# Kernel optimization log

Measured on AMD Instinct MI355X. Metric: run time of the kernel, lower is better.

## Reference

```python
import jax, jax.numpy as jnp
import numpy as np

# dims (must match input_specs / init_kwargs)
T, B_SZ, K, OBS_LAST = 512, 8, 128, 2
OBS_DIM = K * OBS_LAST          # 256
N_ACTIONS = 64
N_UNITS, N_FEAT = 256, 8
D_INNER = N_UNITS * N_FEAT      # 2048
H, N_STATE = 16, 64             # p_heads, state_size
P = D_INNER // H                # headdim = 128


def setup_inputs() -> dict:
    key = jax.random.key(0)
    ks = jax.random.split(key, 12)
    s = lambda fan_in: 1.0 / np.sqrt(fan_in)
    return {
        "obs": jax.random.normal(ks[0], (T, B_SZ, K, OBS_LAST), jnp.float32),
        # input projection obs_dim -> d_inner
        "W_in": jax.random.normal(ks[1], (OBS_DIM, D_INNER), jnp.float32) * s(OBS_DIM),
        "b_in": jnp.zeros((D_INNER,), jnp.float32),
        # SSD cell params (Mamba2-style)
        "A_log": jnp.log(jnp.linspace(1.0, 16.0, H).astype(jnp.float32)),
        "dt_bias": jnp.full((H,), -2.0, jnp.float32),
        "W_dt": jax.random.normal(ks[2], (D_INNER, H), jnp.float32) * s(D_INNER),
        "W_B": jax.random.normal(ks[3], (D_INNER, H * N_STATE), jnp.float32) * s(D_INNER),
        "W_C": jax.random.normal(ks[4], (D_INNER, H * N_STATE), jnp.float32) * s(D_INNER),
        # SSD output projection d_inner -> n_units
        "W_yo": jax.random.normal(ks[5], (D_INNER, N_UNITS), jnp.float32) * s(D_INNER),
        "b_yo": jnp.zeros((N_UNITS,), jnp.float32),
        # policy head n_units -> n_actions
        "W_head": jax.random.normal(ks[6], (N_UNITS, N_ACTIONS), jnp.float32) * s(N_UNITS),
        "b_head": jnp.zeros((N_ACTIONS,), jnp.float32),
    }


def _ssd_scan(x, A_log, dt_bias, W_dt, W_B, W_C):
    # x: (T, B, D_INNER) -> y: (T, B, D_INNER) via selective state-space scan
    t, b, _ = x.shape
    dt = jax.nn.softplus(jnp.einsum("tbd,dh->tbh", x, W_dt) + dt_bias)   # (T,B,H)
    Bm = jnp.einsum("tbd,dm->tbm", x, W_B).reshape(t, b, H, N_STATE)      # (T,B,H,N)
    Cm = jnp.einsum("tbd,dm->tbm", x, W_C).reshape(t, b, H, N_STATE)      # (T,B,H,N)
    xh = x.reshape(t, b, H, P)                                            # (T,B,H,P)
    decay = jnp.exp(-jnp.exp(A_log)[None, None, :] * dt)                  # (T,B,H)

    def step(h, inp):
        dec_t, dt_t, B_t, C_t, x_t = inp
        # h: (B,H,P,N); rank-1 input update per head
        h = dec_t[:, :, None, None] * h + dt_t[:, :, None, None] * jnp.einsum(
            "bhp,bhn->bhpn", x_t, B_t)
        y = jnp.einsum("bhpn,bhn->bhp", h, C_t)                           # (B,H,P)
        return h, y

    h0 = jnp.zeros((b, H, P, N_STATE), x.dtype)
    _, ys = jax.lax.scan(step, h0, (decay, dt, Bm, Cm, xh))
    return ys.reshape(t, b, D_INNER)


def reference(obs, W_in, b_in, A_log, dt_bias, W_dt, W_B, W_C, W_yo, b_yo, W_head, b_head):
    t, b = obs.shape[0], obs.shape[1]
    flat = obs.reshape(t * b, -1)                                 # (t*B, obs_dim)
    x = jax.nn.relu(flat @ W_in + b_in).reshape(t, b, D_INNER)     # (t,B,d_inner)
    y = _ssd_scan(x, A_log, dt_bias, W_dt, W_B, W_C)               # (t,B,d_inner)
    hid = jnp.einsum("tbd,du->tbu", y, W_yo) + b_yo                # (t,B,n_units)
    z = jax.nn.relu(hid).reshape(t * b, N_UNITS)
    logits = z @ W_head + b_head
    return logits.reshape(t, b, N_ACTIONS)
```

## Files before the change

### kernel.cpp

```cpp
#include <hip/hip_runtime.h>
#include <cstdint>
#include <cstddef>

typedef unsigned short u16;
typedef __attribute__((ext_vector_type(8))) __bf16 bf16x8;
typedef __attribute__((ext_vector_type(4))) float floatx4;

#define T_DIM   512
#define B_SZ    8
#define ROWS    4096
#define OBS_D   256
#define D_IN    2048
#define NHEAD   16
#define NSTATE  64
#define PDIM    128
#define NUNITS  256
#define NACT    64
#define NSEG    4
#define SEGT    128
#define SLOT    (B_SZ * NHEAD * PDIM * NSTATE)
#define BCSTR   2176
#define BCN     2048

__host__ __device__ __forceinline__ float bf2f(u16 u) {
    union { uint32_t i; float f; } v; v.i = ((uint32_t)u) << 16; return v.f;
}
__host__ __device__ __forceinline__ u16 f2bf(float f) {
    union { float f; uint32_t i; } v; v.f = f;
    uint32_t r = v.i + 0x7FFFu + ((v.i >> 16) & 1u);
    return (u16)(r >> 16);
}

__device__ __forceinline__ void glds16(const u16* g, u16* l) {
    __builtin_amdgcn_global_load_lds(
        (__attribute__((address_space(1))) void*)g,
        (__attribute__((address_space(3))) void*)l, 16, 0, 0);
}

__global__ __launch_bounds__(256) void ActorAgent_27625229647898_kernel(
        float* __restrict__ out, int n, float v) {
    for (int i = blockIdx.x * 256 + threadIdx.x; i < n; i += gridDim.x * 256)
        out[i] = v;
}

__global__ __launch_bounds__(256) void prep(const float* __restrict__ obs,
                                            const float* __restrict__ W_dt,
                                            const float* __restrict__ W_in,
                                            const float* __restrict__ W_B,
                                            const float* __restrict__ W_C,
                                            const float* __restrict__ W_yo,
                                            const float* __restrict__ W_head,
                                            u16* __restrict__ obsb,
                                            u16* __restrict__ WinT, u16* __restrict__ WBCT,
                                            u16* __restrict__ WdtT,
                                            u16* __restrict__ WyoT, u16* __restrict__ WheadT) {
    int bid = blockIdx.x;
    if (bid < 160) {
        const int NOBS = ROWS * OBS_D;
        const int NDT  = D_IN * NHEAD;
        for (int i = bid * 256 + threadIdx.x; i < NOBS + NDT; i += 160 * 256) {
            if (i < NOBS) obsb[i] = f2bf(obs[i]);
            else {
                int j = i - NOBS;
                int k = j >> 4, n = j & 15;
                WdtT[n * D_IN + k] = f2bf(W_dt[j]);
            }
        }
        return;
    }
    bid -= 160;
    const float* src; u16* dst; int R, C, bx, by;
    if (bid < 512)       { src = W_in;   dst = WinT;   R = 256;  C = 2048; bx = bid & 63; by = bid >> 6; }
    else if (bid < 2560) { int i = bid - 512;  src = W_B;  dst = WBCT; R = 2048; C = 1024; bx = i & 31; by = i >> 5; }
    else if (bid < 4608) { int i = bid - 2560; src = W_C;  dst = WBCT + (size_t)1024 * 2048; R = 2048; C = 1024; bx = i & 31; by = i >> 5; }
    else if (bid < 5120) { int i = bid - 4608; src = W_yo; dst = WyoT; R = 2048; C = 256;  bx = i & 7;  by = i >> 3; }
    else                 { int i = bid - 5120; src = W_head; dst = WheadT; R = 256; C = 64; bx = i & 1; by = i >> 1; }
    __shared__ float t[32][33];
    int c0 = bx * 32, r0 = by * 32;
    int tx = threadIdx.x & 31, ty = threadIdx.x >> 5;
#pragma unroll
    for (int i = 0; i < 32; i += 8)
        t[ty + i][tx] = src[(size_t)(r0 + ty + i) * C + c0 + tx];
    __syncthreads();
#pragma unroll
    for (int i = 0; i < 32; i += 8)
        dst[(size_t)(c0 + ty + i) * R + r0 + tx] = f2bf(t[tx][ty + i]);
}

template <int ACT, int OUT_BF16, int HAS_BIAS>
__global__ __launch_bounds__(256) void gemm_bt128(const u16* __restrict__ A,
                                                  const u16* __restrict__ BT,
                                                  const float* __restrict__ bias,
                                                  void* __restrict__ Cout,
                                                  int M, int N, int K, int ldc) {
    __shared__ __align__(16) u16 sA[128 * 32];
    __shared__ __align__(16) u16 sB[128 * 32];
    const int tid  = threadIdx.x;
    const int wave = tid >> 6, lane = tid & 63;
    const int quad = lane >> 4, lr = lane & 15;
    const int wm = wave & 1, wn = wave >> 1;
    const int m0 = blockIdx.x * 128, n0 = blockIdx.y * 128;
    const int r0 = wave * 32 + (lane >> 2);
    const int kel = (lane & 3) * 8;

    floatx4 acc[4][4];
#pragma unroll
    for (int i = 0; i < 4; i++)
#pragma unroll
        for (int j = 0; j < 4; j++)
#pragma unroll
            for (int r = 0; r < 4; r++) acc[i][j][r] = 0.f;

    const u16* apg = A + (size_t)(m0 + r0) * K + kel;
    const u16* bpg = BT + (size_t)(n0 + r0) * K + kel;
    u16* lA0 = &sA[(wave * 32) * 32];
    u16* lA1 = &sA[(wave * 32 + 16) * 32];
    u16* lB0 = &sB[(wave * 32) * 32];
    u16* lB1 = &sB[(wave * 32 + 16) * 32];

    for (int k0 = 0; k0 < K; k0 += 32) {
        __syncthreads();
        glds16(apg + k0, lA0);
        glds16(apg + (size_t)16 * K + k0, lA1);
        glds16(bpg + k0, lB0);
        glds16(bpg + (size_t)16 * K + k0, lB1);
        __syncthreads();
        bf16x8 af[4], bfr[4];
#pragma unroll
        for (int i = 0; i < 4; i++)
            af[i] = *(const bf16x8*)&sA[(wm * 64 + i * 16 + lr) * 32 + quad * 8];
#pragma unroll
        for (int j = 0; j < 4; j++)
            bfr[j] = *(const bf16x8*)&sB[(wn * 64 + j * 16 + lr) * 32 + quad * 8];
#pragma unroll
        for (int i = 0; i < 4; i++)
#pragma unroll
            for (int j = 0; j < 4; j++)
                acc[i][j] = __builtin_amdgcn_mfma_f32_16x16x32_bf16(af[i], bfr[j], acc[i][j], 0, 0, 0);
    }
#pragma unroll
    for (int j = 0; j < 4; j++) {
        int col = n0 + wn * 64 + j * 16 + lr;
        float bvv = HAS_BIAS ? bias[col] : 0.f;
#pragma unroll
        for (int i = 0; i < 4; i++) {
#pragma unroll
            for (int r = 0; r < 4; r++) {
                int row = m0 + wm * 64 + i * 16 + quad * 4 + r;
                float v = acc[i][j][r] + bvv;
                if (ACT) v = fmaxf(v, 0.f);
                if (OUT_BF16) ((u16*)Cout)[(size_t)row * ldc + col] = f2bf(v);
                else          ((float*)Cout)[(size_t)row * ldc + col] = v;
            }
        }
    }
}

template <int ACT, int OUT_BF16>
__global__ __launch_bounds__(256) void gemm_bt64(const u16* __restrict__ A,
                                                 const u16* __restrict__ BT,
                                                 const float* __restrict__ bias,
                                                 void* __restrict__ Cout,
                                                 int M, int N, int K) {
    __shared__ __align__(16) u16 sA[64 * 64];
    __shared__ __align__(16) u16 sB[64 * 64];
    const int tid  = threadIdx.x;
    const int wave = tid >> 6, lane = tid & 63;
    const int quad = lane >> 4, lr = lane & 15;
    const int m0 = blockIdx.x * 64, n0 = blockIdx.y * 64;
    const int srl = lane >> 3, sc = (lane & 7) * 8;

    floatx4 acc[4];
#pragma unroll
    for (int i = 0; i < 4; i++)
#pragma unroll
        for (int j = 0; j < 4; j++) acc[i][j] = 0.f;

    const u16* apg = A + (size_t)(m0 + wave * 16 + srl) * K + sc;
    const u16* bpg = BT + (size_t)(n0 + wave * 16 + srl) * K + sc;

    for (int k0 = 0; k0 < K; k0 += 64) {
        __syncthreads();
#pragma unroll
        for (int g = 0; g < 2; ++g) {
            glds16(apg + (size_t)(g * 8) * K + k0, &sA[(wave * 16 + g * 8) * 64]);
            glds16(bpg + (size_t)(g * 8) * K + k0, &sB[(wave * 16 + g * 8) * 64]);
        }
        __syncthreads();
#pragma unroll
        for (int ks = 0; ks < 2; ++ks) {
            bf16x8 af = *(const bf16x8*)&sA[(wave * 16 + lr) * 64 + ks * 32 + quad * 8];
#pragma unroll
            for (int nt = 0; nt < 4; nt++) {
                bf16x8 bf = *(const bf16x8*)&sB[(nt * 16 + lr) * 64 + ks * 32 + quad * 8];
                acc[nt] = __builtin_amdgcn_mfma_f32_16x16x32_bf16(af, bf, acc[nt], 0, 0, 0);
            }
        }
    }
#pragma unroll
    for (int nt = 0; nt < 4; nt++) {
        int col = n0 + nt * 16 + lr;
        float bvv = bias ? bias[col] : 0.f;
#pragma unroll
        for (int r = 0; r < 4; r++) {
            int row = m0 + wave * 16 + quad * 4 + r;
            float v = acc[nt][r] + bvv;
            if (ACT) v = fmaxf(v, 0.f);
            if (OUT_BF16) ((u16*)Cout)[(size_t)row * N + col] = f2bf(v);
            else          ((float*)Cout)[(size_t)row * N + col] = v;
        }
    }
}

__global__ __launch_bounds__(512) void dtdecay(const u16* __restrict__ xb,
                                               const u16* __restrict__ WdtT,
                                               const float* __restrict__ dt_bias,
                                               const float* __restrict__ A_log,
                                               float* __restrict__ dtv,
                                               float* __restrict__ decayv) {
    __shared__ __align__(16) u16 sw[NHEAD * D_IN];
    const int tid = threadIdx.x;
#pragma unroll
    for (int i = 0; i < 8; ++i) {
        int idx = (tid + i * 512) * 8;
        *(uint4*)&sw[idx] = *(const uint4*)(WdtT + idx);
    }
    __syncthreads();
    const int wave = tid >> 6, lane = tid & 63;
    const int q = lane >> 4, lr = lane & 15;
    const int row = blockIdx.x * 8 + wave;
    const u16* xp = xb + (size_t)row * D_IN;
    float acc[4] = {0.f, 0.f, 0.f, 0.f};
#pragma unroll 4
    for (int k0 = 0; k0 < 16; ++k0) {
        const int kk = k0 * 128 + lr * 8;
        uint4 xv = *(const uint4*)(xp + kk);
        const u16* xu = (const u16*)&xv;
        float xf[8];
#pragma unroll
        for (int j = 0; j < 8; ++j) xf[j] = bf2f(xu[j]);
#pragma unroll
        for (int j = 0; j < 4; ++j) {
            uint4 wv = *(const uint4*)&sw[(q * 4 + j) * D_IN + kk];
            const u16* wu = (const u16*)&wv;
#pragma unroll
            for (int jj = 0; jj < 8; ++jj)
                acc[j] = fmaf(xf[jj], bf2f(wu[jj]), acc[j]);
        }
    }
#pragma unroll
    for (int m = 1; m <= 8; m <<= 1)
#pragma unroll
        for (int j = 0; j < 4; ++j) acc[j] += __shfl_xor(acc[j], m);
    if (lr == 0) {
#pragma unroll
        for (int j = 0; j < 4; ++j) {
            int h = q * 4 + j;
            float z = acc[j] + dt_bias[h];
            float sp = (z > 20.f) ? z : log1pf(expf(z));
            int o = row * NHEAD + h;
            dtv[o] = sp;
            decayv[o] = expf(-expf(A_log[h]) * sp);
        }
    }
}

__global__ __launch_bounds__(256) void seg_state(const u16* __restrict__ xw,
                                                 const u16* __restrict__ BCm,
                                                 const float* __restrict__ dtv,
                                                 const float* __restrict__ decayv,
                                                 float* __restrict__ Hbuf) {
    const int blk = blockIdx.x;
    const int seg = blk >> 7;
    const int b   = (blk >> 4) & 7;
    const int h   = blk & 15;
    const int tid = threadIdx.x;
    const int pgrp = tid >> 3;
    const int oct  = tid & 7;

    __shared__ __align__(16) u16 sx[SEGT][PDIM];
    __shared__ __align__(16) u16 sbm[SEGT][NSTATE];
    __shared__ float sw[SEGT];
    __shared__ float sdt[SEGT];
    __shared__ float sdec[SEGT];
    __shared__ float sP[32];

    const int t0 = seg * SEGT;

#pragma unroll
    for (int k = 0; k < 8; ++k) {
        int idx = tid + k * 256;
        int t = idx >> 4, c = (idx & 15) * 8;
        int r = (t0 + t) * B_SZ + b;
        *(uint4*)&sx[t][c] = *(const uint4*)(xw + (size_t)r * D_IN + h * PDIM + c);
    }
#pragma unroll
    for (int k = 0; k < 4; ++k) {
        int idx = tid + k * 256;
        int t = idx >> 3, c = (idx & 7) * 8;
        int r = (t0 + t) * B_SZ + b;
        *(uint4*)&sbm[t][c] = *(const uint4*)(BCm + (size_t)r * BCSTR + h * NSTATE + c);
    }
    if (tid < SEGT)            sdt[tid] = dtv[((t0 + tid) * B_SZ + b) * NHEAD + h];
    else if (tid < 2 * SEGT)   sdec[tid - SEGT] = decayv[((t0 + tid - SEGT) * B_SZ + b) * NHEAD + h];
    __syncthreads();

    if (tid < 32) {
        float p = 1.f;
        for (int i = 3; i >= 0; --i) {
            int t = tid * 4 + i;
            sw[t] = sdt[t] * p;
            p *= sdec[t];
        }
        sP[tid] = p;
    }
    __syncthreads();
    if (tid == 0) {
        float suf = 1.f;
        for (int q = 31; q >= 0; --q) { float tmp = sP[q]; sP[q] = suf; suf *= tmp; }
    }
    __syncthreads();
    if (tid < 32) {
        float m = sP[tid];
        for (int i = 0; i < 4; ++i) sw[tid * 4 + i] *= m;
    }
    __syncthreads();

    float acc[4][8];
#pragma unroll
    for (int i = 0; i < 4; i++)
#pragma unroll
        for (int j = 0; j < 8; j++) acc[i][j] = 0.f;

    for (int t = 0; t < SEGT; ++t) {
        float w = sw[t];
        const u16* xp = &sx[t][pgrp * 4];
        const u16* bp = &sbm[t][oct * 8];
        float xv[4], bv[8];
#pragma unroll
        for (int i = 0; i < 4; i++) xv[i] = w * bf2f(xp[i]);
#pragma unroll
        for (int j = 0; j < 8; j++) bv[j] = bf2f(bp[j]);
#pragma unroll
        for (int i = 0; i < 4; i++)
#pragma unroll
            for (int j = 0; j < 8; j++)
                acc[i][j] = fmaf(xv[i], bv[j], acc[i][j]);
    }

    float* base = Hbuf + (size_t)seg * SLOT +
                  (((size_t)b * NHEAD + h) * PDIM + pgrp * 4) * NSTATE + oct * 8;
#pragma unroll
    for (int i = 0; i < 4; i++) {
        *(float4*)(base + (size_t)i * NSTATE)     = make_float4(acc[i][0], acc[i][1], acc[i][2], acc[i][3]);
        *(float4*)(base + (size_t)i * NSTATE + 4) = make_float4(acc[i][4], acc[i][5], acc[i][6], acc[i][7]);
    }
}

__global__ __launch_bounds__(256) void seg_prefix(const float* __restrict__ Hbuf,
                                                  const float* __restrict__ decayv,
                                                  u16* __restrict__ Hbf) {
    const int blk = blockIdx.x;
    const int b  = blk >> 6;
    const int h  = (blk >> 2) & 15;
    const int ec = blk & 3;
    const int tid = threadIdx.x;

    __shared__ float sA[NSEG];

    if (tid < 64 * (NSEG - 2)) {
        int s = 1 + (tid >> 6);
        int i = tid & 63;
        int t = s * SEGT + i * 2;
        float p = decayv[(t * B_SZ + b) * NHEAD + h] *
                  decayv[((t + 1) * B_SZ + b) * NHEAD + h];
        p *= __shfl_xor(p, 1);
        p *= __shfl_xor(p, 2);
        p *= __shfl_xor(p, 4);
        p *= __shfl_xor(p, 8);
        p *= __shfl_xor(p, 16);
        p *= __shfl_xor(p, 32);
        if (i == 0) sA[s] = p;
    }
    __syncthreads();

    const size_t base = (((size_t)b * NHEAD + h) * PDIM * NSTATE) + (size_t)ec * 2048 + tid * 8;
    float4 P0 = *(const float4*)(Hbuf + base);
    float4 P1 = *(const float4*)(Hbuf + base + 4);
    u16 pk[8];
    pk[0] = f2bf(P0.x); pk[1] = f2bf(P0.y); pk[2] = f2bf(P0.z); pk[3] = f2bf(P0.w);
    pk[4] = f2bf(P1.x); pk[5] = f2bf(P1.y); pk[6] = f2bf(P1.z); pk[7] = f2bf(P1.w);
    *(uint4*)(Hbf + base) = *(const uint4*)pk;
#pragma unroll
    for (int s = 1; s <= NSEG - 2; ++s) {
        float a = sA[s];
        const float* slot = Hbuf + (size_t)s * SLOT + base;
        float4 h0 = *(const float4*)(slot);
        float4 h1 = *(const float4*)(slot + 4);
        P0.x = fmaf(a, P0.x, h0.x); P0.y = fmaf(a, P0.y, h0.y);
        P0.z = fmaf(a, P0.z, h0.z); P0.w = fmaf(a, P0.w, h0.w);
        P1.x = fmaf(a, P1.x, h1.x); P1.y = fmaf(a, P1.y, h1.y);
        P1.z = fmaf(a, P1.z, h1.z); P1.w = fmaf(a, P1.w, h1.w);
        pk[0] = f2bf(P0.x); pk[1] = f2bf(P0.y); pk[2] = f2bf(P0.z); pk[3] = f2bf(P0.w);
        pk[4] = f2bf(P1.x); pk[5] = f2bf(P1.y); pk[6] = f2bf(P1.z); pk[7] = f2bf(P1.w);
        *(uint4*)(Hbf + (size_t)s * SLOT + base) = *(const uint4*)pk;
    }
}

__global__ __launch_bounds__(256) void chunk_scan(const u16* __restrict__ BCm,
                                                  const float* __restrict__ dtv,
                                                  const float* __restrict__ decayv,
                                                  const u16* __restrict__ Hbf,
                                                  u16* __restrict__ xb) {
    __shared__ __align__(16) u16 sB_[128][68];
    __shared__ __align__(16) u16 sC_[128][68];
    __shared__ __align__(16) u16 sS[128][132];
    __shared__ __align__(16) u16 sXT[128][36];
    __shared__ float sdt[SEGT], sL[SEGT], sEL[SEGT], stmp[32];

    const int blk = blockIdx.x;
    const int seg = blk >> 7, b = (blk >> 4) & 7, h = blk & 15;
    const int tid = threadIdx.x;
    const int wave = tid >> 6, lane = tid & 63;
    const int quad = lane >> 4, lr = lane & 15;
    const int wm = wave & 1, wn = wave >> 1;
    const int t0 = seg * SEGT;

#pragma unroll
    for (int it = 0; it < 4; ++it) {
        int idx = tid + it * 256;
        int t = idx >> 3, c = (idx & 7) * 8;
        int r = (t0 + t) * B_SZ + b;
        *(uint4*)&sB_[t][c] = *(const uint4*)(BCm + (size_t)r * BCSTR + h * NSTATE + c);
        *(uint4*)&sC_[t][c] = *(const uint4*)(BCm + (size_t)r * BCSTR + 1024 + h * NSTATE + c);
    }
    if (tid < SEGT) sdt[tid] = dtv[((t0 + tid) * B_SZ + b) * NHEAD + h];
    else if (tid < 2 * SEGT) {
        int t = tid - SEGT;
        sL[t] = __logf(fmaxf(decayv[((t0 + t) * B_SZ + b) * NHEAD + h], 1e-30f));
    }
    __syncthreads();
    if (tid < 32) {
        float s = 0.f, v[4];
#pragma unroll
        for (int i = 0; i < 4; ++i) { s += sL[tid * 4 + i]; v[i] = s; }
        stmp[tid] = s;
#pragma unroll
        for (int i = 0; i < 4; ++i) sL[tid * 4 + i] = v[i];
    }
    __syncthreads();
    if (tid == 0) {
        float run = 0.f;
        for (int q = 0; q < 32; ++q) { float c2 = stmp[q]; stmp[q] = run; run += c2; }
    }
    __syncthreads();
    if (tid < 32) {
        float off = stmp[tid];
#pragma unroll
        for (int i = 0; i < 4; ++i) sL[tid * 4 + i] += off;
    }
    __syncthreads();
    if (tid < SEGT) sEL[tid] = __expf(sL[tid]);

    floatx4 accS[4][4];
#pragma unroll
    for (int i = 0; i < 4; i++)
#pragma unroll
        for (int j = 0; j < 4; j++)
#pragma unroll
            for (int r = 0; r < 4; r++) accS[i][j][r] = 0.f;
#pragma unroll
    for (int k0 = 0; k0 < 64; k0 += 32) {
        bf16x8 af[4], bfr[4];
#pragma unroll
        for (int i = 0; i < 4; i++)
            af[i] = *(const bf16x8*)&sB_[wm * 64 + i * 16 + lr][k0 + quad * 8];
#pragma unroll
        for (int j = 0; j < 4; j++)
            bfr[j] = *(const bf16x8*)&sC_[wn * 64 + j * 16 + lr][k0 + quad * 8];
#pragma unroll
        for (int i = 0; i < 4; i++)
#pragma unroll
            for (int j = 0; j < 4; j++)
                accS[i][j] = __builtin_amdgcn_mfma_f32_16x16x32_bf16(af[i], bfr[j], accS[i][j], 0, 0, 0);
    }
#pragma unroll
    for (int j = 0; j < 4; j++) {
        int tt = wn * 64 + j * 16 + lr;
        float Lt = sL[tt];
#pragma unroll
        for (int i = 0; i < 4; i++) {
#pragma unroll
            for (int r = 0; r < 4; r++) {
                int tp = wm * 64 + i * 16 + quad * 4 + r;
                float v = 0.f;
                if (tp <= tt) v = accS[i][j][r] * sdt[tp] * __expf(Lt - sL[tp]);
                sS[tt][tp] = f2bf(v);
            }
        }
    }

    floatx4 acc[4][4];
#pragma unroll
    for (int i = 0; i < 4; i++)
#pragma unroll
        for (int j = 0; j < 4; j++)
#pragma unroll
            for (int r = 0; r < 4; r++) acc[i][j][r] = 0.f;
    __syncthreads();
    if (seg > 0) {
        const u16* hbase = Hbf + (size_t)(seg - 1) * SLOT + (((size_t)b * NHEAD + h) * PDIM) * NSTATE;
#pragma unroll
        for (int k0 = 0; k0 < 64; k0 += 32) {
            bf16x8 af[4], bfr[4];
#pragma unroll
            for (int i = 0; i < 4; i++)
                af[i] = *(const bf16x8*)&sC_[wm * 64 + i * 16 + lr][k0 + quad * 8];
#pragma unroll
            for (int j = 0; j < 4; j++)
                bfr[j] = *(const bf16x8*)(hbase + (size_t)(wn * 64 + j * 16 + lr) * NSTATE + k0 + quad * 8);
#pragma unroll
            for (int i = 0; i < 4; i++)
#pragma unroll
                for (int j = 0; j < 4; j++)
                    acc[i][j] = __builtin_amdgcn_mfma_f32_16x16x32_bf16(af[i], bfr[j], acc[i][j], 0, 0, 0);
        }
#pragma unroll
        for (int i = 0; i < 4; i++) {
#pragma unroll
            for (int r = 0; r < 4; r++) {
                float el = sEL[wm * 64 + i * 16 + quad * 4 + r];
#pragma unroll
                for (int j = 0; j < 4; j++) acc[i][j][r] *= el;
            }
        }
    }

    const int px = tid & 127, koh = (tid >> 7) * 16;
    for (int kc = 0; kc < 128; kc += 32) {
        u16 xv[16];
#pragma unroll
        for (int j2 = 0; j2 < 16; ++j2) {
            int tp = kc + koh + j2;
            xv[j2] = xb[(size_t)((t0 + tp) * B_SZ + b) * D_IN + h * PDIM + px];
        }
        __syncthreads();
        *(uint4*)&sXT[px][koh]     = *(const uint4*)&xv[0];
        *(uint4*)&sXT[px][koh + 8] = *(const uint4*)&xv[8];
        __syncthreads();
        bf16x8 af[4], bfr[4];
#pragma unroll
        for (int i = 0; i < 4; i++)
            af[i] = *(const bf16x8*)&sS[wm * 64 + i * 16 + lr][kc + quad * 8];
#pragma unroll
        for (int j = 0; j < 4; j++)
            bfr[j] = *(const bf16x8*)&sXT[wn * 64 + j * 16 + lr][quad * 8];
#pragma unroll
        for (int i = 0; i < 4; i++)
#pragma unroll
            for (int j = 0; j < 4; j++)
                acc[i][j] = __builtin_amdgcn_mfma_f32_16x16x32_bf16(af[i], bfr[j], acc[i][j], 0, 0, 0);
    }

#pragma unroll
    for (int j = 0; j < 4; j++) {
        int p = wn * 64 + j * 16 + lr;
#pragma unroll
        for (int i = 0; i < 4; i++) {
#pragma unroll
            for (int r = 0; r < 4; r++) {
                int t = wm * 64 + i * 16 + quad * 4 + r;
                xb[(size_t)((t0 + t) * B_SZ + b) * D_IN + h * PDIM + p] = f2bf(acc[i][j][r]);
            }
        }
    }
}

extern "C" void kernel_launch(void* const* d_in, const int* in_sizes, int n_in,
                              void* d_out, int out_size, void* d_ws, size_t ws_size,
                              hipStream_t stream) {
    const float* obs     = (const float*)d_in[0];
    const float* W_in    = (const float*)d_in[1];
    const float* b_in    = (const float*)d_in[2];
    const float* A_log   = (const float*)d_in[3];
    const float* dt_bias = (const float*)d_in[4];
    const float* W_dt    = (const float*)d_in[5];
    const float* W_B     = (const float*)d_in[6];
    const float* W_C     = (const float*)d_in[7];
    const float* W_yo    = (const float*)d_in[8];
    const float* b_yo    = (const float*)d_in[9];
    const float* W_head  = (const float*)d_in[10];
    const float* b_head  = (const float*)d_in[11];

    char* ws = (char*)d_ws;
    size_t o = 0;
    u16*   xb     = (u16*)(ws + o);   o += (size_t)ROWS * D_IN * 2;
    u16*   BCm    = (u16*)(ws + o);   o += (size_t)ROWS * BCSTR * 2;
    float* dtv    = (float*)(ws + o); o += (size_t)ROWS * NHEAD * 4;
    float* decayv = (float*)(ws + o); o += (size_t)ROWS * NHEAD * 4;
    u16*   zb     = (u16*)(ws + o);   o += (size_t)ROWS * NUNITS * 2;
    float* Hseg   = (float*)(ws + o); o += (size_t)(NSEG - 1) * SLOT * 4;
    u16*   Hbf    = (u16*)(ws + o);   o += (size_t)(NSEG - 1) * SLOT * 2;
    u16*   obsb   = (u16*)(ws + o);   o += (size_t)ROWS * OBS_D * 2;
    u16*   WinT   = (u16*)(ws + o);   o += (size_t)D_IN * OBS_D * 2;
    u16*   WBCT   = (u16*)(ws + o);   o += (size_t)BCN * D_IN * 2;
    u16*   WdtT   = (u16*)(ws + o);   o += (size_t)NHEAD * D_IN * 2;
    u16*   WyoT   = (u16*)(ws + o);   o += (size_t)NUNITS * D_IN * 2;
    u16*   WheadT = (u16*)(ws + o);   o += (size_t)NACT * NUNITS * 2;

    ActorAgent_27625229647898_kernel<<<dim3(1), 256, 0, stream>>>((float*)d_out, 0, 0.f);

    prep<<<dim3(160 + 5136), 256, 0, stream>>>(obs, W_dt, W_in, W_B, W_C, W_yo, W_head,
                                               obsb, WinT, WBCT, WdtT, WyoT, WheadT);

    gemm_bt128<1, 1, 1><<<dim3(32, 16), 256, 0, stream>>>(obsb, WinT, b_in, xb, ROWS, D_IN, OBS_D, D_IN);
    dtdecay<<<dim3(512), 512, 0, stream>>>(xb, WdtT, dt_bias, A_log, dtv, decayv);
    gemm_bt128<0, 1, 0><<<dim3(32, 16), 256, 0, stream>>>(xb, WBCT, (const float*)nullptr, BCm, ROWS, BCN, D_IN, BCSTR);
    seg_state<<<dim3((NSEG - 1) * 128), 256, 0, stream>>>(xb, BCm, dtv, decayv, Hseg);
    seg_prefix<<<dim3(512), 256, 0, stream>>>(Hseg, decayv, Hbf);
    chunk_scan<<<dim3(NSEG * 128), 256, 0, stream>>>(BCm, dtv, decayv, Hbf, xb);
    gemm_bt64<1, 1><<<dim3(64, 4), 256, 0, stream>>>(xb, WyoT, b_yo, zb, ROWS, NUNITS, D_IN);
    gemm_bt64<0, 0><<<dim3(64, 1), 256, 0, stream>>>(zb, WheadT, b_head, (float*)d_out, ROWS, NACT, NUNITS);
}
```

Measured before the change: 256.4 us.

## Double-buffer LDS tiles in GEMMs and process two rows per wave in dtdecay

Both bf16 MFMA GEMM kernels now use ping-pong LDS buffers. The next K-tile is issued via global-to-LDS loads before computing on the current tile, with one waitcnt plus barrier per iteration instead of two syncthreads. This aims to overlap global load latency with MFMA work, at the cost of twice the LDS per block. Separately, dtdecay has each wave handle two rows and launches half as many blocks, amortizing the 64KB shared weight load per block.

```diff
diff --git a/kernel.cpp b/kernel.cpp
--- a/kernel.cpp
+++ b/kernel.cpp
@@ -93,8 +93,8 @@
                                                   const float* __restrict__ bias,
                                                   void* __restrict__ Cout,
                                                   int M, int N, int K, int ldc) {
-    __shared__ __align__(16) u16 sA[128 * 32];
-    __shared__ __align__(16) u16 sB[128 * 32];
+    __shared__ __align__(16) u16 sA[2][128 * 32];
+    __shared__ __align__(16) u16 sB[2][128 * 32];
     const int tid  = threadIdx.x;
     const int wave = tid >> 6, lane = tid & 63;
     const int quad = lane >> 4, lr = lane & 15;
@@ -113,30 +113,39 @@
 
     const u16* apg = A + (size_t)(m0 + r0) * K + kel;
     const u16* bpg = BT + (size_t)(n0 + r0) * K + kel;
-    u16* lA0 = &sA[(wave * 32) * 32];
-    u16* lA1 = &sA[(wave * 32 + 16) * 32];
-    u16* lB0 = &sB[(wave * 32) * 32];
-    u16* lB1 = &sB[(wave * 32 + 16) * 32];
-
+    const int lofs = (wave * 32) * 32;
+
+    glds16(apg, &sA[0][lofs]);
+    glds16(apg + (size_t)16 * K, &sA[0][lofs + 16 * 32]);
+    glds16(bpg, &sB[0][lofs]);
+    glds16(bpg + (size_t)16 * K, &sB[0][lofs + 16 * 32]);
+    asm volatile("s_waitcnt vmcnt(0)" ::: "memory");
+    __builtin_amdgcn_s_barrier();
+
+    int cur = 0;
     for (int k0 = 0; k0 < K; k0 += 32) {
-        __syncthreads();
-        glds16(apg + k0, lA0);
-        glds16(apg + (size_t)16 * K + k0, lA1);
-        glds16(bpg + k0, lB0);
-        glds16(bpg + (size_t)16 * K + k0, lB1);
-        __syncthreads();
+        if (k0 + 32 < K) {
+            int nb = cur ^ 1;
+            glds16(apg + k0 + 32, &sA[nb][lofs]);
+            glds16(apg + (size_t)16 * K + k0 + 32, &sA[nb][lofs + 16 * 32]);
+            glds16(bpg + k0 + 32, &sB[nb][lofs]);
+            glds16(bpg + (size_t)16 * K + k0 + 32, &sB[nb][lofs + 16 * 32]);
+        }
         bf16x8 af[4], bfr[4];
 #pragma unroll
         for (int i = 0; i < 4; i++)
-            af[i] = *(const bf16x8*)&sA[(wm * 64 + i * 16 + lr) * 32 + quad * 8];
+            af[i] = *(const bf16x8*)&sA[cur][(wm * 64 + i * 16 + lr) * 32 + quad * 8];
 #pragma unroll
         for (int j = 0; j < 4; j++)
-            bfr[j] = *(const bf16x8*)&sB[(wn * 64 + j * 16 + lr) * 32 + quad * 8];
+            bfr[j] = *(const bf16x8*)&sB[cur][(wn * 64 + j * 16 + lr) * 32 + quad * 8];
 #pragma unroll
         for (int i = 0; i < 4; i++)
 #pragma unroll
             for (int j = 0; j < 4; j++)
                 acc[i][j] = __builtin_amdgcn_mfma_f32_16x16x32_bf16(af[i], bfr[j], acc[i][j], 0, 0, 0);
+        asm volatile("s_waitcnt vmcnt(0)" ::: "memory");
+        __builtin_amdgcn_s_barrier();
+        cur ^= 1;
     }
 #pragma unroll
     for (int j = 0; j < 4; j++) {
@@ -162,8 +171,8 @@
                                                  const float* __restrict__ bias,
                                                  void* __restrict__ Cout,
                                                  int M, int N, int K) {
-    __shared__ __align__(16) u16 sA[64 * 64];
-    __shared__ __align__(16) u16 sB[64 * 64];
+    __shared__ __align__(16) u16 sA[2][64 * 64];
+    __shared__ __align__(16) u16 sB[2][64 * 64];
     const int tid  = threadIdx.x;
     const int wave = tid >> 6, lane = tid & 63;
     const int quad = lane >> 4, lr = lane & 15;
@@ -179,23 +188,36 @@
     const u16* apg = A + (size_t)(m0 + wave * 16 + srl) * K + sc;
     const u16* bpg = BT + (size_t)(n0 + wave * 16 + srl) * K + sc;
 
+#pragma unroll
+    for (int g = 0; g < 2; ++g) {
+        glds16(apg + (size_t)(g * 8) * K, &sA[0][(wave * 16 + g * 8) * 64]);
+        glds16(bpg + (size_t)(g * 8) * K, &sB[0][(wave * 16 + g * 8) * 64]);
+    }
+    asm volatile("s_waitcnt vmcnt(0)" ::: "memory");
+    __builtin_amdgcn_s_barrier();
+
+    int cur = 0;
     for (int k0 = 0; k0 < K; k0 += 64) {
-        __syncthreads();
-#pragma unroll
-        for (int g = 0; g < 2; ++g) {
-            glds16(apg + (size_t)(g * 8) * K + k0, &sA[(wave * 16 + g * 8) * 64]);
-            glds16(bpg + (size_t)(g * 8) * K + k0, &sB[(wave * 16 + g * 8) * 64]);
-        }
-        __syncthreads();
+        if (k0 + 64 < K) {
+            int nb = cur ^ 1;
+#pragma unroll
+            for (int g = 0; g < 2; ++g) {
+                glds16(apg + (size_t)(g * 8) * K + k0 + 64, &sA[nb][(wave * 16 + g * 8) * 64]);
+                glds16(bpg + (size_t)(g * 8) * K + k0 + 64, &sB[nb][(wave * 16 + g * 8) * 64]);
+            }
+        }
 #pragma unroll
         for (int ks = 0; ks < 2; ++ks) {
-            bf16x8 af = *(const bf16x8*)&sA[(wave * 16 + lr) * 64 + ks * 32 + quad * 8];
+            bf16x8 af = *(const bf16x8*)&sA[cur][(wave * 16 + lr) * 64 + ks * 32 + quad * 8];
 #pragma unroll
             for (int nt = 0; nt < 4; nt++) {
-                bf16x8 bf = *(const bf16x8*)&sB[(nt * 16 + lr) * 64 + ks * 32 + quad * 8];
+                bf16x8 bf = *(const bf16x8*)&sB[cur][(nt * 16 + lr) * 64 + ks * 32 + quad * 8];
                 acc[nt] = __builtin_amdgcn_mfma_f32_16x16x32_bf16(af, bf, acc[nt], 0, 0, 0);
             }
         }
+        asm volatile("s_waitcnt vmcnt(0)" ::: "memory");
+        __builtin_amdgcn_s_barrier();
+        cur ^= 1;
     }
 #pragma unroll
     for (int nt = 0; nt < 4; nt++) {
@@ -228,39 +250,42 @@
     __syncthreads();
     const int wave = tid >> 6, lane = tid & 63;
     const int q = lane >> 4, lr = lane & 15;
-    const int row = blockIdx.x * 8 + wave;
-    const u16* xp = xb + (size_t)row * D_IN;
-    float acc[4] = {0.f, 0.f, 0.f, 0.f};
+#pragma unroll 1
+    for (int rr = 0; rr < 2; ++rr) {
+        const int row = blockIdx.x * 16 + wave * 2 + rr;
+        const u16* xp = xb + (size_t)row * D_IN;
+        float acc[4] = {0.f, 0.f, 0.f, 0.f};
 #pragma unroll 4
-    for (int k0 = 0; k0 < 16; ++k0) {
-        const int kk = k0 * 128 + lr * 8;
-        uint4 xv = *(const uint4*)(xp + kk);
-        const u16* xu = (const u16*)&xv;
-        float xf[8];
-#pragma unroll
-        for (int j = 0; j < 8; ++j) xf[j] = bf2f(xu[j]);
-#pragma unroll
-        for (int j = 0; j < 4; ++j) {
-            uint4 wv = *(const uint4*)&sw[(q * 4 + j) * D_IN + kk];
-            const u16* wu = (const u16*)&wv;
-#pragma unroll
-            for (int jj = 0; jj < 8; ++jj)
-                acc[j] = fmaf(xf[jj], bf2f(wu[jj]), acc[j]);
-        }
-    }
-#pragma unroll
-    for (int m = 1; m <= 8; m <<= 1)
-#pragma unroll
-        for (int j = 0; j < 4; ++j) acc[j] += __shfl_xor(acc[j], m);
-    if (lr == 0) {
-#pragma unroll
-        for (int j = 0; j < 4; ++j) {
-            int h = q * 4 + j;
-            float z = acc[j] + dt_bias[h];
-            float sp = (z > 20.f) ? z : log1pf(expf(z));
-            int o = row * NHEAD + h;
-            dtv[o] = sp;
-            decayv[o] = expf(-expf(A_log[h]) * sp);
+        for (int k0 = 0; k0 < 16; ++k0) {
+            const int kk = k0 * 128 + lr * 8;
+            uint4 xv = *(const uint4*)(xp + kk);
+            const u16* xu = (const u16*)&xv;
+            float xf[8];
+#pragma unroll
+            for (int j = 0; j < 8; ++j) xf[j] = bf2f(xu[j]);
+#pragma unroll
+            for (int j = 0; j < 4; ++j) {
+                uint4 wv = *(const uint4*)&sw[(q * 4 + j) * D_IN + kk];
+                const u16* wu = (const u16*)&wv;
+#pragma unroll
+                for (int jj = 0; jj < 8; ++jj)
+                    acc[j] = fmaf(xf[jj], bf2f(wu[jj]), acc[j]);
+            }
+        }
+#pragma unroll
+        for (int m = 1; m <= 8; m <<= 1)
+#pragma unroll
+            for (int j = 0; j < 4; ++j) acc[j] += __shfl_xor(acc[j], m);
+        if (lr == 0) {
+#pragma unroll
+            for (int j = 0; j < 4; ++j) {
+                int h = q * 4 + j;
+                float z = acc[j] + dt_bias[h];
+                float sp = (z > 20.f) ? z : log1pf(expf(z));
+                int o = row * NHEAD + h;
+                dtv[o] = sp;
+                decayv[o] = expf(-expf(A_log[h]) * sp);
+            }
         }
     }
 }
@@ -614,7 +639,7 @@
                                                obsb, WinT, WBCT, WdtT, WyoT, WheadT);
 
     gemm_bt128<1, 1, 1><<<dim3(32, 16), 256, 0, stream>>>(obsb, WinT, b_in, xb, ROWS, D_IN, OBS_D, D_IN);
-    dtdecay<<<dim3(512), 512, 0, stream>>>(xb, WdtT, dt_bias, A_log, dtv, decayv);
+    dtdecay<<<dim3(256), 512, 0, stream>>>(xb, WdtT, dt_bias, A_log, dtv, decayv);
     gemm_bt128<0, 1, 0><<<dim3(32, 16), 256, 0, stream>>>(xb, WBCT, (const float*)nullptr, BCm, ROWS, BCN, D_IN, BCSTR);
     seg_state<<<dim3((NSEG - 1) * 128), 256, 0, stream>>>(xb, BCm, dtv, decayv, Hseg);
     seg_prefix<<<dim3(512), 256, 0, stream>>>(Hseg, decayv, Hbf);
```

Result: no change. 255.1 us (-0.5%).

## Triple-buffer GEMM LDS loads and process two rows per wave in dtdecay

Applied to the files above, without the earlier changes.

Both GEMM kernels move to a three-stage LDS ring. Global-to-LDS loads are issued two k-tiles ahead and guarded by explicit vmcnt waits and raw barriers, so memory latency overlaps with the MFMA work. The dtdecay kernel now has each wave compute two rows, which reuses each shared-memory weight read and halves the grid. This costs more LDS per block, which may lower occupancy, and the hand-placed waitcnt counts assume each glds16 issues exactly one vm op.

```diff
diff --git a/kernel.cpp b/kernel.cpp
--- a/kernel.cpp
+++ b/kernel.cpp
@@ -93,8 +93,8 @@
                                                   const float* __restrict__ bias,
                                                   void* __restrict__ Cout,
                                                   int M, int N, int K, int ldc) {
-    __shared__ __align__(16) u16 sA[128 * 32];
-    __shared__ __align__(16) u16 sB[128 * 32];
+    __shared__ __align__(16) u16 sA[3][128 * 32];
+    __shared__ __align__(16) u16 sB[3][128 * 32];
     const int tid  = threadIdx.x;
     const int wave = tid >> 6, lane = tid & 63;
     const int quad = lane >> 4, lr = lane & 15;
@@ -113,31 +113,49 @@
 
     const u16* apg = A + (size_t)(m0 + r0) * K + kel;
     const u16* bpg = BT + (size_t)(n0 + r0) * K + kel;
-    u16* lA0 = &sA[(wave * 32) * 32];
-    u16* lA1 = &sA[(wave * 32 + 16) * 32];
-    u16* lB0 = &sB[(wave * 32) * 32];
-    u16* lB1 = &sB[(wave * 32 + 16) * 32];
-
-    for (int k0 = 0; k0 < K; k0 += 32) {
-        __syncthreads();
-        glds16(apg + k0, lA0);
-        glds16(apg + (size_t)16 * K + k0, lA1);
-        glds16(bpg + k0, lB0);
-        glds16(bpg + (size_t)16 * K + k0, lB1);
-        __syncthreads();
+    const int lofs = (wave * 32) * 32;
+    const int ntk = K >> 5;
+
+#define STAGE128(t, sb) do {                                        \
+        int kk_ = (t) << 5;                                         \
+        glds16(apg + kk_, &sA[sb][lofs]);                           \
+        glds16(apg + (size_t)16 * K + kk_, &sA[sb][lofs + 16 * 32]);\
+        glds16(bpg + kk_, &sB[sb][lofs]);                           \
+        glds16(bpg + (size_t)16 * K + kk_, &sB[sb][lofs + 16 * 32]);\
+    } while (0)
+
+    STAGE128(0, 0);
+    STAGE128(1, 1);
+    int s = 0;
+    for (int t = 0; t < ntk; ++t) {
+        if (t + 2 < ntk) {
+            int ns = s + 2; if (ns >= 3) ns -= 3;
+            STAGE128(t + 2, ns);
+            asm volatile("s_waitcnt vmcnt(8)" ::: "memory");
+        } else if (t + 1 < ntk) {
+            asm volatile("s_waitcnt vmcnt(4)" ::: "memory");
+        } else {
+            asm volatile("s_waitcnt vmcnt(0)" ::: "memory");
+        }
+        __builtin_amdgcn_s_barrier();
+        asm volatile("" ::: "memory");
         bf16x8 af[4], bfr[4];
 #pragma unroll
         for (int i = 0; i < 4; i++)
-            af[i] = *(const bf16x8*)&sA[(wm * 64 + i * 16 + lr) * 32 + quad * 8];
+            af[i] = *(const bf16x8*)&sA[s][(wm * 64 + i * 16 + lr) * 32 + quad * 8];
 #pragma unroll
         for (int j = 0; j < 4; j++)
-            bfr[j] = *(const bf16x8*)&sB[(wn * 64 + j * 16 + lr) * 32 + quad * 8];
+            bfr[j] = *(const bf16x8*)&sB[s][(wn * 64 + j * 16 + lr) * 32 + quad * 8];
 #pragma unroll
         for (int i = 0; i < 4; i++)
 #pragma unroll
             for (int j = 0; j < 4; j++)
                 acc[i][j] = __builtin_amdgcn_mfma_f32_16x16x32_bf16(af[i], bfr[j], acc[i][j], 0, 0, 0);
-    }
+        asm volatile("" ::: "memory");
+        __builtin_amdgcn_s_barrier();
+        ++s; if (s == 3) s = 0;
+    }
+#undef STAGE128
 #pragma unroll
     for (int j = 0; j < 4; j++) {
         int col = n0 + wn * 64 + j * 16 + lr;
@@ -162,8 +180,8 @@
                                                  const float* __restrict__ bias,
                                                  void* __restrict__ Cout,
                                                  int M, int N, int K) {
-    __shared__ __align__(16) u16 sA[64 * 64];
-    __shared__ __align__(16) u16 sB[64 * 64];
+    __shared__ __align__(16) u16 sA[3][64 * 64];
+    __shared__ __align__(16) u16 sB[3][64 * 64];
     const int tid  = threadIdx.x;
     const int wave = tid >> 6, lane = tid & 63;
     const int quad = lane >> 4, lr = lane & 15;
@@ -178,25 +196,45 @@
 
     const u16* apg = A + (size_t)(m0 + wave * 16 + srl) * K + sc;
     const u16* bpg = BT + (size_t)(n0 + wave * 16 + srl) * K + sc;
-
-    for (int k0 = 0; k0 < K; k0 += 64) {
-        __syncthreads();
-#pragma unroll
-        for (int g = 0; g < 2; ++g) {
-            glds16(apg + (size_t)(g * 8) * K + k0, &sA[(wave * 16 + g * 8) * 64]);
-            glds16(bpg + (size_t)(g * 8) * K + k0, &sB[(wave * 16 + g * 8) * 64]);
-        }
-        __syncthreads();
+    const int ntk = K >> 6;
+
+#define STAGE64(t, sb) do {                                            \
+        int kk_ = (t) << 6;                                            \
+        glds16(apg + kk_,                 &sA[sb][(wave * 16) * 64]);  \
+        glds16(apg + (size_t)8 * K + kk_, &sA[sb][(wave * 16 + 8) * 64]);\
+        glds16(bpg + kk_,                 &sB[sb][(wave * 16) * 64]);  \
+        glds16(bpg + (size_t)8 * K + kk_, &sB[sb][(wave * 16 + 8) * 64]);\
+    } while (0)
+
+    STAGE64(0, 0);
+    STAGE64(1, 1);
+    int s = 0;
+    for (int t = 0; t < ntk; ++t) {
+        if (t + 2 < ntk) {
+            int ns = s + 2; if (ns >= 3) ns -= 3;
+            STAGE64(t + 2, ns);
+            asm volatile("s_waitcnt vmcnt(8)" ::: "memory");
+        } else if (t + 1 < ntk) {
+            asm volatile("s_waitcnt vmcnt(4)" ::: "memory");
+        } else {
+            asm volatile("s_waitcnt vmcnt(0)" ::: "memory");
+        }
+        __builtin_amdgcn_s_barrier();
+        asm volatile("" ::: "memory");
 #pragma unroll
         for (int ks = 0; ks < 2; ++ks) {
-            bf16x8 af = *(const bf16x8*)&sA[(wave * 16 + lr) * 64 + ks * 32 + quad * 8];
+            bf16x8 af = *(const bf16x8*)&sA[s][(wave * 16 + lr) * 64 + ks * 32 + quad * 8];
 #pragma unroll
             for (int nt = 0; nt < 4; nt++) {
-                bf16x8 bf = *(const bf16x8*)&sB[(nt * 16 + lr) * 64 + ks * 32 + quad * 8];
+                bf16x8 bf = *(const bf16x8*)&sB[s][(nt * 16 + lr) * 64 + ks * 32 + quad * 8];
                 acc[nt] = __builtin_amdgcn_mfma_f32_16x16x32_bf16(af, bf, acc[nt], 0, 0, 0);
             }
         }
-    }
+        asm volatile("" ::: "memory");
+        __builtin_amdgcn_s_barrier();
+        ++s; if (s == 3) s = 0;
+    }
+#undef STAGE64
 #pragma unroll
     for (int nt = 0; nt < 4; nt++) {
         int col = n0 + nt * 16 + lr;
@@ -228,39 +266,53 @@
     __syncthreads();
     const int wave = tid >> 6, lane = tid & 63;
     const int q = lane >> 4, lr = lane & 15;
-    const int row = blockIdx.x * 8 + wave;
-    const u16* xp = xb + (size_t)row * D_IN;
-    float acc[4] = {0.f, 0.f, 0.f, 0.f};
+    const int row0 = blockIdx.x * 16 + wave * 2;
+    const u16* xp0 = xb + (size_t)row0 * D_IN;
+    const u16* xp1 = xb + (size_t)(row0 + 1) * D_IN;
+    float acc0[4] = {0.f, 0.f, 0.f, 0.f};
+    float acc1[4] = {0.f, 0.f, 0.f, 0.f};
 #pragma unroll 4
     for (int k0 = 0; k0 < 16; ++k0) {
         const int kk = k0 * 128 + lr * 8;
-        uint4 xv = *(const uint4*)(xp + kk);
-        const u16* xu = (const u16*)&xv;
-        float xf[8];
-#pragma unroll
-        for (int j = 0; j < 8; ++j) xf[j] = bf2f(xu[j]);
+        uint4 xv0 = *(const uint4*)(xp0 + kk);
+        uint4 xv1 = *(const uint4*)(xp1 + kk);
+        const u16* xu0 = (const u16*)&xv0;
+        const u16* xu1 = (const u16*)&xv1;
+        float xf0[8], xf1[8];
+#pragma unroll
+        for (int j = 0; j < 8; ++j) { xf0[j] = bf2f(xu0[j]); xf1[j] = bf2f(xu1[j]); }
 #pragma unroll
         for (int j = 0; j < 4; ++j) {
             uint4 wv = *(const uint4*)&sw[(q * 4 + j) * D_IN + kk];
             const u16* wu = (const u16*)&wv;
 #pragma unroll
-            for (int jj = 0; jj < 8; ++jj)
-                acc[j] = fmaf(xf[jj], bf2f(wu[jj]), acc[j]);
+            for (int jj = 0; jj < 8; ++jj) {
+                float wf = bf2f(wu[jj]);
+                acc0[j] = fmaf(xf0[jj], wf, acc0[j]);
+                acc1[j] = fmaf(xf1[jj], wf, acc1[j]);
+            }
         }
     }
 #pragma unroll
     for (int m = 1; m <= 8; m <<= 1)
 #pragma unroll
-        for (int j = 0; j < 4; ++j) acc[j] += __shfl_xor(acc[j], m);
+        for (int j = 0; j < 4; ++j) {
+            acc0[j] += __shfl_xor(acc0[j], m);
+            acc1[j] += __shfl_xor(acc1[j], m);
+        }
     if (lr == 0) {
 #pragma unroll
         for (int j = 0; j < 4; ++j) {
             int h = q * 4 + j;
-            float z = acc[j] + dt_bias[h];
-            float sp = (z > 20.f) ? z : log1pf(expf(z));
-            int o = row * NHEAD + h;
-            dtv[o] = sp;
-            decayv[o] = expf(-expf(A_log[h]) * sp);
+            float ae = expf(A_log[h]);
+            float z0 = acc0[j] + dt_bias[h];
+            float sp0 = (z0 > 20.f) ? z0 : log1pf(expf(z0));
+            float z1 = acc1[j] + dt_bias[h];
+            float sp1 = (z1 > 20.f) ? z1 : log1pf(expf(z1));
+            dtv[row0 * NHEAD + h] = sp0;
+            decayv[row0 * NHEAD + h] = expf(-ae * sp0);
+            dtv[(row0 + 1) * NHEAD + h] = sp1;
+            decayv[(row0 + 1) * NHEAD + h] = expf(-ae * sp1);
         }
     }
 }
@@ -614,7 +666,7 @@
                                                obsb, WinT, WBCT, WdtT, WyoT, WheadT);
 
     gemm_bt128<1, 1, 1><<<dim3(32, 16), 256, 0, stream>>>(obsb, WinT, b_in, xb, ROWS, D_IN, OBS_D, D_IN);
-    dtdecay<<<dim3(512), 512, 0, stream>>>(xb, WdtT, dt_bias, A_log, dtv, decayv);
+    dtdecay<<<dim3(256), 512, 0, stream>>>(xb, WdtT, dt_bias, A_log, dtv, decayv);
     gemm_bt128<0, 1, 0><<<dim3(32, 16), 256, 0, stream>>>(xb, WBCT, (const float*)nullptr, BCm, ROWS, BCN, D_IN, BCSTR);
     seg_state<<<dim3((NSEG - 1) * 128), 256, 0, stream>>>(xb, BCm, dtv, decayv, Hseg);
     seg_prefix<<<dim3(512), 256, 0, stream>>>(Hseg, decayv, Hbf);
```

New measurement: 247.5 us. 1.04x faster.
